# Optimization experiments

Hardware: AMD Instinct MI355X
Metric: run time of the kernel (lower is better)

Reference implementation:

```python
import jax, jax.numpy as jnp
import numpy as np

N_HEADS = 4
TAU = 0.1

def _ln(x, w, b):
    m = jnp.mean(x, axis=-1, keepdims=True)
    v = jnp.mean(jnp.square(x - m), axis=-1, keepdims=True)
    return (x - m) / jnp.sqrt(v + 1e-6) * w + b

def _l2norm(x):
    # torch F.normalize(dim=1): x / max(||x||_2, 1e-12)
    n = jnp.linalg.norm(x, axis=1, keepdims=True)
    return x / jnp.maximum(n, 1e-12)

def _sincos_pe(T, dim):
    pos = jnp.arange(T, dtype=jnp.float32)[:, None]
    div = jnp.exp(jnp.arange(0, dim, 2, dtype=jnp.float32) * (-np.log(10000.0) / dim))
    ang = pos * div[None, :]
    # interleave: even indices sin, odd indices cos
    return jnp.stack([jnp.sin(ang), jnp.cos(ang)], axis=-1).reshape(T, dim)

def reference(x, p1_w, p1_b, pln1_w, pln1_b, p2_w, pln2_w, pln2_b,
              in_proj_w, in_proj_b, out_proj_w, out_proj_b,
              ln1_w, ln1_b, lin1_w, lin1_b, lin2_w, lin2_b, ln2_w, ln2_b, head_w):
    B, T, D = x.shape
    E = p2_w.shape[0]           # bottleneck_dim = 256
    H = N_HEADS
    hd = E // H
    # projector: Linear -> LN -> GELU -> Linear(no bias) -> LN
    h = jax.nn.gelu(_ln(x.reshape(B * T, D) @ p1_w.T + p1_b, pln1_w, pln1_b), approximate=False)
    h = _ln(h @ p2_w.T, pln2_w, pln2_b).reshape(B, T, E)
    h = h + _sincos_pe(T, E)[None]
    causal = jnp.tril(jnp.ones((T, T), dtype=bool))
    L = in_proj_w.shape[0]
    for i in range(L):  # post-norm TransformerEncoderLayer
        qkv = h @ in_proj_w[i].T + in_proj_b[i]        # [B,T,3E]
        q, k, v = jnp.split(qkv, 3, axis=-1)
        q = q.reshape(B, T, H, hd).transpose(0, 2, 1, 3)
        k = k.reshape(B, T, H, hd).transpose(0, 2, 1, 3)
        v = v.reshape(B, T, H, hd).transpose(0, 2, 1, 3)
        scores = jnp.einsum('bhtd,bhsd->bhts', q, k) / np.float32(np.sqrt(hd))
        scores = jnp.where(causal[None, None], scores, -jnp.inf)
        probs = jax.nn.softmax(scores, axis=-1)        # materialized attn probs (eager path)
        attn = jnp.einsum('bhts,bhsd->bhtd', probs, v).transpose(0, 2, 1, 3).reshape(B, T, E)
        attn = attn @ out_proj_w[i].T + out_proj_b[i]
        h = _ln(h + attn, ln1_w[i], ln1_b[i])
        ff = jax.nn.gelu(h @ lin1_w[i].T + lin1_b[i], approximate=False) @ lin2_w[i].T + lin2_b[i]
        h = _ln(h + ff, ln2_w[i], ln2_b[i])
    flat = _l2norm(h.reshape(B * T, E))
    wn = _l2norm(head_w)
    return (flat @ wn.T / TAU).reshape(B, T, -1)

def setup_inputs() -> dict:
    key = jax.random.key(0)
    ks = jax.random.split(key, 8)
    B, T, D, E, HID, CLS, L = 2048, 20, 2048, 256, 1024, 1000, 2
    s = 0.02
    def w(k, shape):
        return jax.random.normal(k, shape, jnp.float32) * s
    return {
        'x': jax.random.normal(ks[0], (B, T, D), jnp.float32),
        'p1_w': w(ks[1], (HID, D)), 'p1_b': jnp.zeros((HID,), jnp.float32),
        'pln1_w': jnp.ones((HID,), jnp.float32), 'pln1_b': jnp.zeros((HID,), jnp.float32),
        'p2_w': w(ks[2], (E, HID)),
        'pln2_w': jnp.ones((E,), jnp.float32), 'pln2_b': jnp.zeros((E,), jnp.float32),
        'in_proj_w': w(ks[3], (L, 3 * E, E)), 'in_proj_b': jnp.zeros((L, 3 * E), jnp.float32),
        'out_proj_w': w(ks[4], (L, E, E)), 'out_proj_b': jnp.zeros((L, E), jnp.float32),
        'ln1_w': jnp.ones((L, E), jnp.float32), 'ln1_b': jnp.zeros((L, E), jnp.float32),
        'lin1_w': w(ks[5], (L, 4 * E, E)), 'lin1_b': jnp.zeros((L, 4 * E), jnp.float32),
        'lin2_w': w(ks[6], (L, E, 4 * E)), 'lin2_b': jnp.zeros((L, E), jnp.float32),
        'ln2_w': jnp.ones((L, E), jnp.float32), 'ln2_b': jnp.zeros((L, E), jnp.float32),
        'head_w': w(ks[7], (CLS, E)),
    }
```

## Files before the change

kernel.cpp:

```cpp
#include <hip/hip_runtime.h>
#include <math.h>

#define CDIV(a,b) (((a)+(b)-1)/(b))

typedef unsigned short bfu;
typedef short   s16x8 __attribute__((ext_vector_type(8)));
typedef float   f32x4 __attribute__((ext_vector_type(4)));

#define GLOAD16(gp, lp) __builtin_amdgcn_global_load_lds( \
    (const __attribute__((address_space(1))) void*)(gp),  \
    (__attribute__((address_space(3))) void*)(lp), 16, 0, 0)

static __device__ __forceinline__ float gelu_exact(float x) {
    return 0.5f * x * (1.0f + erff(x * 0.7071067811865475f));
}
static __device__ __forceinline__ bfu f2bf(float x) {
    unsigned int u = __float_as_uint(x);
    unsigned int r = u + 0x7fffu + ((u >> 16) & 1u);
    return (bfu)(r >> 16);
}
static __device__ __forceinline__ float bf2f(bfu b) {
    return __uint_as_float(((unsigned int)b) << 16);
}
static __device__ __forceinline__ float wave_sum(float v) {
    #pragma unroll
    for (int off = 32; off; off >>= 1) v += __shfl_xor(v, off, 64);
    return v;
}

__global__ __launch_bounds__(256)
void cvt_kernel(const float* __restrict__ in, bfu* __restrict__ out, int n4)
{
    int i = blockIdx.x * 256 + threadIdx.x;
    const int stride = gridDim.x * 256;
    for (; i < n4; i += stride) {
        float4 f = ((const float4*)in)[i];
        ushort4 o;
        o.x = f2bf(f.x); o.y = f2bf(f.y); o.z = f2bf(f.z); o.w = f2bf(f.w);
        ((ushort4*)out)[i] = o;
    }
}

__global__ __launch_bounds__(256)
void cvt6_kernel(const float* __restrict__ s0, const float* __restrict__ s1,
                 const float* __restrict__ s2, const float* __restrict__ s3,
                 const float* __restrict__ s4, const float* __restrict__ s5,
                 bfu* __restrict__ dst)
{
    const int c0 = 524288;
    const int c1 = c0 + 65536;
    const int c2 = c1 + 98304;
    const int c3 = c2 + 32768;
    const int c4 = c3 + 131072;
    const int c5 = c4 + 131072;
    int i = blockIdx.x * 256 + threadIdx.x;
    const int stride = gridDim.x * 256;
    for (; i < c5; i += stride) {
        const float* s; int base;
        if      (i < c0) { s = s0; base = 0;  }
        else if (i < c1) { s = s1; base = c0; }
        else if (i < c2) { s = s2; base = c1; }
        else if (i < c3) { s = s3; base = c2; }
        else if (i < c4) { s = s4; base = c3; }
        else             { s = s5; base = c4; }
        float4 f = ((const float4*)s)[i - base];
        ushort4 o;
        o.x = f2bf(f.x); o.y = f2bf(f.y); o.z = f2bf(f.z); o.w = f2bf(f.w);
        ((ushort4*)dst)[i] = o;
    }
}

__global__ __launch_bounds__(256)
void pe_kernel(float* __restrict__ pe)
{
    const int t = blockIdx.x;
    const int c = threadIdx.x;
    const float div = expf((float)(c & ~1) * (-9.210340371976184f / 256.0f));
    const float ang = (float)t * div;
    pe[t * 256 + c] = (c & 1) ? cosf(ang) : sinf(ang);
}

template<bool GELU_EP, bool OUT_BF16>
__global__ __launch_bounds__(256)
void mfma_gemm(const bfu* __restrict__ A, const bfu* __restrict__ W,
               const float* __restrict__ bias, void* __restrict__ Cv,
               int M, int N, int K, float scale, int ntx)
{
    __shared__ bfu As[128 * 32];
    __shared__ bfu Ws[128 * 32];

    const int tid = threadIdx.x;
    const int nwg = gridDim.x;
    const int lid = (nwg & 7) ? (int)blockIdx.x
                              : ((int)blockIdx.x & 7) * (nwg >> 3) + ((int)blockIdx.x >> 3);
    const int row0 = (lid / ntx) * 128;
    const int col0 = (lid % ntx) * 128;

    const int lane = tid & 63;
    const int wave = tid >> 6;
    const int wm = (wave >> 1) * 64;
    const int wn = (wave & 1) * 64;
    const int fr = lane & 15;
    const int fk = (lane >> 4) * 8;

    const int lrow = lane >> 2;
    const int lk   = (lane & 3) * 8;
    const bfu* al0 = A + (size_t)(row0 + wave * 32 + lrow) * K + lk;
    const bfu* al1 = al0 + (size_t)16 * K;
    const bfu* wl0 = W + (size_t)(col0 + wave * 32 + lrow) * K + lk;
    const bfu* wl1 = wl0 + (size_t)16 * K;
    bfu* ad0 = &As[(wave * 2    ) * 512];
    bfu* ad1 = &As[(wave * 2 + 1) * 512];
    bfu* wd0 = &Ws[(wave * 2    ) * 512];
    bfu* wd1 = &Ws[(wave * 2 + 1) * 512];

    f32x4 acc[4][4];
    #pragma unroll
    for (int i = 0; i < 4; ++i)
        #pragma unroll
        for (int j = 0; j < 4; ++j) acc[i][j] = (f32x4)0.f;

    for (int k0 = 0; k0 < K; k0 += 32) {
        GLOAD16(al0 + k0, ad0);
        GLOAD16(al1 + k0, ad1);
        GLOAD16(wl0 + k0, wd0);
        GLOAD16(wl1 + k0, wd1);
        __syncthreads();

        s16x8 af[4], wf[4];
        #pragma unroll
        for (int i = 0; i < 4; ++i) af[i] = *(const s16x8*)&As[(wm + 16*i + fr) * 32 + fk];
        #pragma unroll
        for (int j = 0; j < 4; ++j) wf[j] = *(const s16x8*)&Ws[(wn + 16*j + fr) * 32 + fk];

        #pragma unroll
        for (int i = 0; i < 4; ++i)
            #pragma unroll
            for (int j = 0; j < 4; ++j)
                acc[i][j] = __builtin_amdgcn_mfma_f32_16x16x32_bf16(af[i], wf[j], acc[i][j], 0, 0, 0);
        __syncthreads();
    }

    #pragma unroll
    for (int i = 0; i < 4; ++i) {
        const int r = row0 + wm + 16 * i + (lane >> 4) * 4;
        #pragma unroll
        for (int j = 0; j < 4; ++j) {
            const int c = col0 + wn + 16 * j + fr;
            if (c < N) {
                const float bsum = bias ? bias[c] : 0.f;
                #pragma unroll
                for (int rr = 0; rr < 4; ++rr) {
                    float v = acc[i][j][rr] + bsum;
                    if (GELU_EP) v = gelu_exact(v);
                    v *= scale;
                    if (OUT_BF16) ((bfu*)Cv)[(size_t)(r + rr) * N + c] = f2bf(v);
                    else          ((float*)Cv)[(size_t)(r + rr) * N + c] = v;
                }
            }
        }
    }
}

template<bool GELU_EP, bool OUT_BF16>
__global__ __launch_bounds__(512, 2)
void mfma_gemm256(const bfu* __restrict__ A, const bfu* __restrict__ W,
                  const float* __restrict__ bias, void* __restrict__ Cv,
                  int M, int N, int K, float scale, int ntx)
{
    __shared__ bfu lds[2][2][8192];

    const int tid  = threadIdx.x;
    const int lane = tid & 63;
    const int wv   = tid >> 6;
    const int nwg  = gridDim.x;
    const int lid  = (nwg & 7) ? (int)blockIdx.x
                               : ((int)blockIdx.x & 7) * (nwg >> 3) + ((int)blockIdx.x >> 3);
    const int row0 = (lid / ntx) * 256;
    const int col0 = (lid % ntx) * 256;

    const int srow = wv * 16 + (lane >> 2);
    const int sk   = ((lane & 3) ^ ((lane >> 2) & 3)) * 8;
    const bfu* aS0 = A + (size_t)(row0 + srow)       * K + sk;
    const bfu* aS1 = A + (size_t)(row0 + srow + 128) * K + sk;
    const bfu* wS0 = W + (size_t)(col0 + srow)       * K + sk;
    const bfu* wS1 = W + (size_t)(col0 + srow + 128) * K + sk;
    const int dOff = wv * 512;

    const int wr = wv >> 2, wc = wv & 3;
    const int fr = lane & 15;
    const int slot = (((lane >> 4) ^ (fr & 3))) * 8;

    f32x4 acc[8][4];
    #pragma unroll
    for (int i = 0; i < 8; ++i)
        #pragma unroll
        for (int j = 0; j < 4; ++j) acc[i][j] = (f32x4)0.f;

    const int nt = K >> 5;

#define STAGE256(b_, t_) do { \
    const size_t ko_ = (size_t)(t_) * 32; \
    GLOAD16(aS0 + ko_, &lds[b_][0][dOff]); \
    GLOAD16(aS1 + ko_, &lds[b_][0][4096 + dOff]); \
    GLOAD16(wS0 + ko_, &lds[b_][1][dOff]); \
    GLOAD16(wS1 + ko_, &lds[b_][1][4096 + dOff]); \
} while (0)

    STAGE256(0, 0);
    STAGE256(1, 1);

    int cur = 0;
    for (int t = 0; t < nt; ++t) {
        if (t + 1 < nt) asm volatile("s_waitcnt vmcnt(4)" ::: "memory");
        else            asm volatile("s_waitcnt vmcnt(0)" ::: "memory");
        asm volatile("s_barrier" ::: "memory");

        const bfu* Ab = lds[cur][0];
        const bfu* Wb = lds[cur][1];

        s16x8 bfr[4], afr[8];
        #pragma unroll
        for (int j = 0; j < 4; ++j)
            bfr[j] = *(const s16x8*)&Wb[(wc * 64 + j * 16 + fr) * 32 + slot];
        #pragma unroll
        for (int i = 0; i < 4; ++i)
            afr[i] = *(const s16x8*)&Ab[(wr * 128 + i * 16 + fr) * 32 + slot];

        __builtin_amdgcn_s_setprio(1);
        #pragma unroll
        for (int i = 0; i < 4; ++i)
            #pragma unroll
            for (int j = 0; j < 4; ++j)
                acc[i][j] = __builtin_amdgcn_mfma_f32_16x16x32_bf16(afr[i], bfr[j], acc[i][j], 0, 0, 0);
        __builtin_amdgcn_s_setprio(0);

        #pragma unroll
        for (int i = 4; i < 8; ++i)
            afr[i] = *(const s16x8*)&Ab[(wr * 128 + i * 16 + fr) * 32 + slot];

        __builtin_amdgcn_s_setprio(1);
        #pragma unroll
        for (int i = 4; i < 8; ++i)
            #pragma unroll
            for (int j = 0; j < 4; ++j)
                acc[i][j] = __builtin_amdgcn_mfma_f32_16x16x32_bf16(afr[i], bfr[j], acc[i][j], 0, 0, 0);
        __builtin_amdgcn_s_setprio(0);

        asm volatile("s_barrier" ::: "memory");
        if (t + 2 < nt) STAGE256(cur, t + 2);
        cur ^= 1;
    }
#undef STAGE256

    #pragma unroll
    for (int i = 0; i < 8; ++i) {
        const int r = row0 + wr * 128 + 16 * i + (lane >> 4) * 4;
        #pragma unroll
        for (int j = 0; j < 4; ++j) {
            const int c = col0 + wc * 64 + 16 * j + fr;
            if (c < N) {
                const float bsum = bias ? bias[c] : 0.f;
                #pragma unroll
                for (int rr = 0; rr < 4; ++rr) {
                    float v = acc[i][j][rr] + bsum;
                    if (GELU_EP) v = gelu_exact(v);
                    v *= scale;
                    if (OUT_BF16) ((bfu*)Cv)[(size_t)(r + rr) * N + c] = f2bf(v);
                    else          ((float*)Cv)[(size_t)(r + rr) * N + c] = v;
                }
            }
        }
    }
}

__global__ __launch_bounds__(256)
void ln1024_kernel(const bfu* __restrict__ X, const float* __restrict__ w,
                   const float* __restrict__ b, bfu* __restrict__ Y)
{
    __shared__ float sbuf[4];
    const int row = blockIdx.x;
    const bfu* xr = X + (size_t)row * 1024;

    ushort4 t4 = *(const ushort4*)(xr + threadIdx.x * 4);
    float v[4] = {bf2f(t4.x), bf2f(t4.y), bf2f(t4.z), bf2f(t4.w)};

    float s = v[0] + v[1] + v[2] + v[3];
    s = wave_sum(s);
    const int lane = threadIdx.x & 63, wid = threadIdx.x >> 6;
    if (lane == 0) sbuf[wid] = s;
    __syncthreads();
    const float mean = (sbuf[0] + sbuf[1] + sbuf[2] + sbuf[3]) * (1.f / 1024.f);

    float q = 0.f;
    #pragma unroll
    for (int j = 0; j < 4; ++j) { float d = v[j] - mean; q += d * d; }
    q = wave_sum(q);
    __syncthreads();
    if (lane == 0) sbuf[wid] = q;
    __syncthreads();
    const float var  = (sbuf[0] + sbuf[1] + sbuf[2] + sbuf[3]) * (1.f / 1024.f);
    const float rstd = rsqrtf(var + 1e-6f);

    ushort4 o;
    #pragma unroll
    for (int j = 0; j < 4; ++j) {
        const int c = threadIdx.x * 4 + j;
        float y = gelu_exact((v[j] - mean) * rstd * w[c] + b[c]);
        ((bfu*)&o)[j] = f2bf(y);
    }
    *(ushort4*)(Y + (size_t)row * 1024 + threadIdx.x * 4) = o;
}

template<bool ADD_PE, bool RES>
__global__ __launch_bounds__(256)
void ln256_kernel(const float* __restrict__ X, const float* __restrict__ R,
                  const float* __restrict__ w, const float* __restrict__ b,
                  const float* __restrict__ pe, float* __restrict__ Yf,
                  bfu* __restrict__ Yb, int T)
{
    const int row  = blockIdx.x * 4 + (threadIdx.x >> 6);
    const int lane = threadIdx.x & 63;

    float4 v = *(const float4*)(X + (size_t)row * 256 + lane * 4);
    if (RES) {
        float4 r4 = *(const float4*)(R + (size_t)row * 256 + lane * 4);
        v.x += r4.x; v.y += r4.y; v.z += r4.z; v.w += r4.w;
    }

    const float mean = wave_sum(v.x + v.y + v.z + v.w) * (1.f / 256.f);
    float q = (v.x-mean)*(v.x-mean) + (v.y-mean)*(v.y-mean)
            + (v.z-mean)*(v.z-mean) + (v.w-mean)*(v.w-mean);
    const float rstd = rsqrtf(wave_sum(q) * (1.f / 256.f) + 1e-6f);

    const float4 w4 = *(const float4*)(w + lane * 4);
    const float4 b4 = *(const float4*)(b + lane * 4);
    float y[4] = {(v.x-mean)*rstd*w4.x + b4.x, (v.y-mean)*rstd*w4.y + b4.y,
                  (v.z-mean)*rstd*w4.z + b4.z, (v.w-mean)*rstd*w4.w + b4.w};
    if (ADD_PE) {
        const float4 p4 = *(const float4*)(pe + (size_t)(row % T) * 256 + lane * 4);
        y[0] += p4.x; y[1] += p4.y; y[2] += p4.z; y[3] += p4.w;
    }

    if (Yf) *(float4*)(Yf + (size_t)row * 256 + lane * 4) = float4{y[0], y[1], y[2], y[3]};
    if (Yb) {
        ushort4 o = {f2bf(y[0]), f2bf(y[1]), f2bf(y[2]), f2bf(y[3])};
        *(ushort4*)(Yb + (size_t)row * 256 + lane * 4) = o;
    }
}

__global__ __launch_bounds__(64)
void attn_kernel(const bfu* __restrict__ qkv, bfu* __restrict__ out,
                 int B, int T, int H)
{
    __shared__ float qs[20][65];
    __shared__ float ks[20][65];
    __shared__ float vs[20][65];
    __shared__ float probs[64];

    const int blk = blockIdx.x;
    const int b = blk / H;
    const int h = blk % H;
    const int tid = threadIdx.x;

    for (int t = 0; t < T; ++t) {
        const bfu* base = qkv + (size_t)(b * T + t) * 768 + h * 64 + tid;
        qs[t][tid] = bf2f(base[0]);
        ks[t][tid] = bf2f(base[256]);
        vs[t][tid] = bf2f(base[512]);
    }
    __syncthreads();

    for (int t = 0; t < T; ++t) {
        float sc = -INFINITY;
        if (tid <= t) {
            float s = 0.f;
            #pragma unroll
            for (int d = 0; d < 64; ++d) s = fmaf(qs[t][d], ks[tid][d], s);
            sc = s * 0.125f;
        }
        float m = sc;
        #pragma unroll
        for (int off = 32; off; off >>= 1) m = fmaxf(m, __shfl_xor(m, off, 64));
        float p = (tid <= t) ? expf(sc - m) : 0.f;
        float sum = p;
        #pragma unroll
        for (int off = 32; off; off >>= 1) sum += __shfl_xor(sum, off, 64);
        p /= sum;
        probs[tid] = p;
        __syncthreads();

        float o = 0.f;
        for (int s = 0; s <= t; ++s) o = fmaf(probs[s], vs[s][tid], o);
        out[(size_t)(b * T + t) * 256 + h * 64 + tid] = f2bf(o);
        __syncthreads();
    }
}

__global__ __launch_bounds__(256)
void l2norm_kernel(const float* __restrict__ X, bfu* __restrict__ Y)
{
    const int row  = blockIdx.x * 4 + (threadIdx.x >> 6);
    const int lane = threadIdx.x & 63;
    float4 v = *(const float4*)(X + (size_t)row * 256 + lane * 4);
    float n = sqrtf(wave_sum(v.x*v.x + v.y*v.y + v.z*v.z + v.w*v.w));
    n = 1.f / fmaxf(n, 1e-12f);
    ushort4 o = {f2bf(v.x*n), f2bf(v.y*n), f2bf(v.z*n), f2bf(v.w*n)};
    *(ushort4*)(Y + (size_t)row * 256 + lane * 4) = o;
}

extern "C" void kernel_launch(void* const* d_in, const int* in_sizes, int n_in,
                              void* d_out, int out_size, void* d_ws, size_t ws_size,
                              hipStream_t stream)
{
    const float* x         = (const float*)d_in[0];
    const float* p1_w      = (const float*)d_in[1];
    const float* p1_b      = (const float*)d_in[2];
    const float* pln1_w    = (const float*)d_in[3];
    const float* pln1_b    = (const float*)d_in[4];
    const float* p2_w      = (const float*)d_in[5];
    const float* pln2_w    = (const float*)d_in[6];
    const float* pln2_b    = (const float*)d_in[7];
    const float* in_proj_w = (const float*)d_in[8];
    const float* in_proj_b = (const float*)d_in[9];
    const float* out_proj_w= (const float*)d_in[10];
    const float* out_proj_b= (const float*)d_in[11];
    const float* ln1_w     = (const float*)d_in[12];
    const float* ln1_b     = (const float*)d_in[13];
    const float* lin1_w    = (const float*)d_in[14];
    const float* lin1_b    = (const float*)d_in[15];
    const float* lin2_w    = (const float*)d_in[16];
    const float* lin2_b    = (const float*)d_in[17];
    const float* ln2_w     = (const float*)d_in[18];
    const float* ln2_b     = (const float*)d_in[19];
    const float* head_w    = (const float*)d_in[20];

    const int B = 2048, T = 20, E = 256, HID = 1024, CLS = 1000, L = 2, H = 4;
    const int M = B * T;
    const int D = 2048;

    char* p = (char*)d_ws;
    bfu*   xb     = (bfu*)p;    p += (size_t)M * D * 2;
    bfu*   h1b    = (bfu*)p;    p += (size_t)M * HID * 2;
    bfu*   wblk   = (bfu*)p;    p += (size_t)3932160 * 2;
    bfu*   wnb    = (bfu*)p;    p += (size_t)1024 * E * 2;
    float* pe     = (float*)p;  p += (size_t)T * 256 * 4;

    char* q = (char*)xb;
    float* h      = (float*)q;  q += (size_t)M * E * 4;
    float* ffout  = (float*)q;  q += (size_t)M * E * 4;
    bfu*   hb     = (bfu*)q;    q += (size_t)M * E * 2;
    bfu*   abf    = (bfu*)q;    q += (size_t)M * E * 2;

    bfu* p1wb  = wblk;
    bfu* p2wb  = p1wb  + (size_t)HID * D;
    bfu* qkvwb = p2wb  + (size_t)E * HID;
    bfu* outwb = qkvwb + (size_t)L * 3 * E * E;
    bfu* l1wb  = outwb + (size_t)L * E * E;
    bfu* l2wb  = l1wb  + (size_t)L * 4 * E * E;

    float* out   = (float*)d_out;
    bfu*   qkvb  = (bfu*)d_out;
    float* attnp = (float*)d_out;

    cvt_kernel<<<2048, 256, 0, stream>>>(x, xb, M * D / 4);
    cvt6_kernel<<<2048, 256, 0, stream>>>(p1_w, p2_w, in_proj_w, out_proj_w, lin1_w, lin2_w, wblk);
    pe_kernel<<<T, 256, 0, stream>>>(pe);

    mfma_gemm256<false, true><<<dim3((M/256) * (HID/256)), 512, 0, stream>>>(
        xb, p1wb, p1_b, h1b, M, HID, D, 1.f, HID/256);
    ln1024_kernel<<<M, 256, 0, stream>>>(h1b, pln1_w, pln1_b, h1b);
    mfma_gemm256<false, false><<<dim3(M/256), 512, 0, stream>>>(
        h1b, p2wb, nullptr, h, M, E, HID, 1.f, 1);
    ln256_kernel<true, false><<<M/4, 256, 0, stream>>>(
        h, nullptr, pln2_w, pln2_b, pe, h, hb, T);

    for (int l = 0; l < L; ++l) {
        mfma_gemm<false, true><<<dim3(6 * (M/128)), 256, 0, stream>>>(
            hb, qkvwb + (size_t)l * 3*E*E, in_proj_b + (size_t)l * 3*E, qkvb, M, 3*E, E, 1.f, 6);
        attn_kernel<<<B * H, 64, 0, stream>>>(qkvb, abf, B, T, H);
        mfma_gemm<false, false><<<dim3(2 * (M/128)), 256, 0, stream>>>(
            abf, outwb + (size_t)l * E*E, out_proj_b + (size_t)l * E, attnp, M, E, E, 1.f, 2);
        ln256_kernel<false, true><<<M/4, 256, 0, stream>>>(
            h, attnp, ln1_w + (size_t)l * E, ln1_b + (size_t)l * E, nullptr, h, hb, T);
        mfma_gemm<true, true><<<dim3(8 * (M/128)), 256, 0, stream>>>(
            hb, l1wb + (size_t)l * 4*E*E, lin1_b + (size_t)l * 4*E, h1b, M, HID, E, 1.f, 8);
        mfma_gemm256<false, false><<<dim3(M/256), 512, 0, stream>>>(
            h1b, l2wb + (size_t)l * E*4*E, lin2_b + (size_t)l * E, ffout, M, E, HID, 1.f, 1);
        ln256_kernel<false, true><<<M/4, 256, 0, stream>>>(
            h, ffout, ln2_w + (size_t)l * E, ln2_b + (size_t)l * E, nullptr, h, hb, T);
    }

    l2norm_kernel<<<M/4, 256, 0, stream>>>(h, hb);
    l2norm_kernel<<<CLS/4, 256, 0, stream>>>(head_w, wnb);
    mfma_gemm<false, false><<<dim3(8 * (M/128)), 256, 0, stream>>>(
        hb, wnb, nullptr, out, M, CLS, E, 10.f, 8);
}
```

Baseline: 1.257 ms.

## Fuse residual+LayerNorm into N=256 GEMM epilogues and use 256-tile GEMM everywhere

Adds a GEMM kernel whose block covers 128 full rows of the 256-wide output. Its epilogue adds bias and the residual, reduces mean and variance across waves through LDS, then writes the normalized fp32 and bf16 activations in place. This replaces the separate p2, out_proj and lin2 GEMMs plus their ln256 passes, removing the round trips of the intermediate fp32 buffers. The remaining 128x128 GEMM launches (QKV, lin1, classifier head) move to the double-buffered 256x256 kernel. Risks: variance is now computed as E[x^2]-mean^2, which is less stable, and the grids for the N=256 GEMMs are smaller.

```diff
diff --git a/kernel.cpp b/kernel.cpp
--- a/kernel.cpp
+++ b/kernel.cpp
@@ -81,88 +81,6 @@
 }
 
 template<bool GELU_EP, bool OUT_BF16>
-__global__ __launch_bounds__(256)
-void mfma_gemm(const bfu* __restrict__ A, const bfu* __restrict__ W,
-               const float* __restrict__ bias, void* __restrict__ Cv,
-               int M, int N, int K, float scale, int ntx)
-{
-    __shared__ bfu As[128 * 32];
-    __shared__ bfu Ws[128 * 32];
-
-    const int tid = threadIdx.x;
-    const int nwg = gridDim.x;
-    const int lid = (nwg & 7) ? (int)blockIdx.x
-                              : ((int)blockIdx.x & 7) * (nwg >> 3) + ((int)blockIdx.x >> 3);
-    const int row0 = (lid / ntx) * 128;
-    const int col0 = (lid % ntx) * 128;
-
-    const int lane = tid & 63;
-    const int wave = tid >> 6;
-    const int wm = (wave >> 1) * 64;
-    const int wn = (wave & 1) * 64;
-    const int fr = lane & 15;
-    const int fk = (lane >> 4) * 8;
-
-    const int lrow = lane >> 2;
-    const int lk   = (lane & 3) * 8;
-    const bfu* al0 = A + (size_t)(row0 + wave * 32 + lrow) * K + lk;
-    const bfu* al1 = al0 + (size_t)16 * K;
-    const bfu* wl0 = W + (size_t)(col0 + wave * 32 + lrow) * K + lk;
-    const bfu* wl1 = wl0 + (size_t)16 * K;
-    bfu* ad0 = &As[(wave * 2    ) * 512];
-    bfu* ad1 = &As[(wave * 2 + 1) * 512];
-    bfu* wd0 = &Ws[(wave * 2    ) * 512];
-    bfu* wd1 = &Ws[(wave * 2 + 1) * 512];
-
-    f32x4 acc[4][4];
-    #pragma unroll
-    for (int i = 0; i < 4; ++i)
-        #pragma unroll
-        for (int j = 0; j < 4; ++j) acc[i][j] = (f32x4)0.f;
-
-    for (int k0 = 0; k0 < K; k0 += 32) {
-        GLOAD16(al0 + k0, ad0);
-        GLOAD16(al1 + k0, ad1);
-        GLOAD16(wl0 + k0, wd0);
-        GLOAD16(wl1 + k0, wd1);
-        __syncthreads();
-
-        s16x8 af[4], wf[4];
-        #pragma unroll
-        for (int i = 0; i < 4; ++i) af[i] = *(const s16x8*)&As[(wm + 16*i + fr) * 32 + fk];
-        #pragma unroll
-        for (int j = 0; j < 4; ++j) wf[j] = *(const s16x8*)&Ws[(wn + 16*j + fr) * 32 + fk];
-
-        #pragma unroll
-        for (int i = 0; i < 4; ++i)
-            #pragma unroll
-            for (int j = 0; j < 4; ++j)
-                acc[i][j] = __builtin_amdgcn_mfma_f32_16x16x32_bf16(af[i], wf[j], acc[i][j], 0, 0, 0);
-        __syncthreads();
-    }
-
-    #pragma unroll
-    for (int i = 0; i < 4; ++i) {
-        const int r = row0 + wm + 16 * i + (lane >> 4) * 4;
-        #pragma unroll
-        for (int j = 0; j < 4; ++j) {
-            const int c = col0 + wn + 16 * j + fr;
-            if (c < N) {
-                const float bsum = bias ? bias[c] : 0.f;
-                #pragma unroll
-                for (int rr = 0; rr < 4; ++rr) {
-                    float v = acc[i][j][rr] + bsum;
-                    if (GELU_EP) v = gelu_exact(v);
-                    v *= scale;
-                    if (OUT_BF16) ((bfu*)Cv)[(size_t)(r + rr) * N + c] = f2bf(v);
-                    else          ((float*)Cv)[(size_t)(r + rr) * N + c] = v;
-                }
-            }
-        }
-    }
-}
-
-template<bool GELU_EP, bool OUT_BF16>
 __global__ __launch_bounds__(512, 2)
 void mfma_gemm256(const bfu* __restrict__ A, const bfu* __restrict__ W,
                   const float* __restrict__ bias, void* __restrict__ Cv,
@@ -274,6 +192,153 @@
     }
 }
 
+template<bool RES, bool ADD_PE>
+__global__ __launch_bounds__(512, 2)
+void mfma_gemm_ln(const bfu* __restrict__ A, const bfu* __restrict__ W,
+                  const float* __restrict__ bias, const float* __restrict__ R,
+                  const float* __restrict__ lnw, const float* __restrict__ lnb,
+                  const float* __restrict__ pe, float* __restrict__ Yf,
+                  bfu* __restrict__ Yb, int M, int K, int T)
+{
+    __shared__ bfu ldsA[2][4096];
+    __shared__ bfu ldsW[2][8192];
+
+    const int tid  = threadIdx.x;
+    const int lane = tid & 63;
+    const int wv   = tid >> 6;
+    const int nwg  = gridDim.x;
+    const int lid  = (nwg & 7) ? (int)blockIdx.x
+                               : ((int)blockIdx.x & 7) * (nwg >> 3) + ((int)blockIdx.x >> 3);
+    const int row0 = lid * 128;
+
+    const int srow = wv * 16 + (lane >> 2);
+    const int sk   = ((lane & 3) ^ ((lane >> 2) & 3)) * 8;
+    const bfu* aS  = A + (size_t)(row0 + srow) * K + sk;
+    const bfu* wS0 = W + (size_t)(srow)        * K + sk;
+    const bfu* wS1 = W + (size_t)(srow + 128)  * K + sk;
+    const int dOff = wv * 512;
+
+    const int wr = wv >> 2, wc = wv & 3;
+    const int fr = lane & 15;
+    const int g4 = lane >> 4;
+    const int slot = ((g4 ^ (fr & 3))) * 8;
+
+    f32x4 acc[4][4];
+    #pragma unroll
+    for (int i = 0; i < 4; ++i)
+        #pragma unroll
+        for (int j = 0; j < 4; ++j) acc[i][j] = (f32x4)0.f;
+
+    const int nt = K >> 5;
+
+#define STAGELN(b_, t_) do { \
+    const size_t ko_ = (size_t)(t_) * 32; \
+    GLOAD16(aS  + ko_, &ldsA[b_][dOff]); \
+    GLOAD16(wS0 + ko_, &ldsW[b_][dOff]); \
+    GLOAD16(wS1 + ko_, &ldsW[b_][4096 + dOff]); \
+} while (0)
+
+    STAGELN(0, 0);
+    STAGELN(1, 1);
+
+    int cur = 0;
+    for (int t = 0; t < nt; ++t) {
+        if (t + 1 < nt) asm volatile("s_waitcnt vmcnt(3)" ::: "memory");
+        else            asm volatile("s_waitcnt vmcnt(0)" ::: "memory");
+        asm volatile("s_barrier" ::: "memory");
+
+        const bfu* Ab = ldsA[cur];
+        const bfu* Wb = ldsW[cur];
+
+        s16x8 bfr[4], afr[4];
+        #pragma unroll
+        for (int j = 0; j < 4; ++j)
+            bfr[j] = *(const s16x8*)&Wb[(wc * 64 + j * 16 + fr) * 32 + slot];
+        #pragma unroll
+        for (int i = 0; i < 4; ++i)
+            afr[i] = *(const s16x8*)&Ab[(wr * 64 + i * 16 + fr) * 32 + slot];
+
+        __builtin_amdgcn_s_setprio(1);
+        #pragma unroll
+        for (int i = 0; i < 4; ++i)
+            #pragma unroll
+            for (int j = 0; j < 4; ++j)
+                acc[i][j] = __builtin_amdgcn_mfma_f32_16x16x32_bf16(afr[i], bfr[j], acc[i][j], 0, 0, 0);
+        __builtin_amdgcn_s_setprio(0);
+
+        asm volatile("s_barrier" ::: "memory");
+        if (t + 2 < nt) STAGELN(cur, t + 2);
+        cur ^= 1;
+    }
+#undef STAGELN
+
+    float* red   = (float*)ldsA;
+    float* stats = red + 1024;
+
+    float bj[4];
+    #pragma unroll
+    for (int j = 0; j < 4; ++j)
+        bj[j] = bias ? bias[wc * 64 + j * 16 + fr] : 0.f;
+
+    #pragma unroll
+    for (int i = 0; i < 4; ++i) {
+        #pragma unroll
+        for (int rr = 0; rr < 4; ++rr) {
+            const int rl = wr * 64 + i * 16 + g4 * 4 + rr;
+            const size_t r = (size_t)(row0 + rl);
+            float s = 0.f, q = 0.f;
+            #pragma unroll
+            for (int j = 0; j < 4; ++j) {
+                float v = acc[i][j][rr] + bj[j];
+                if (RES) v += R[r * 256 + (wc * 64 + j * 16 + fr)];
+                acc[i][j][rr] = v;
+                s += v; q += v * v;
+            }
+            #pragma unroll
+            for (int off = 1; off < 16; off <<= 1) {
+                s += __shfl_xor(s, off, 64);
+                q += __shfl_xor(q, off, 64);
+            }
+            if (fr == 0) { red[rl * 4 + wc] = s; red[512 + rl * 4 + wc] = q; }
+        }
+    }
+    __syncthreads();
+    if (tid < 128) {
+        const float s = red[tid*4+0] + red[tid*4+1] + red[tid*4+2] + red[tid*4+3];
+        const float q = red[512+tid*4+0] + red[512+tid*4+1] + red[512+tid*4+2] + red[512+tid*4+3];
+        const float mean = s * (1.f / 256.f);
+        const float var  = q * (1.f / 256.f) - mean * mean;
+        stats[tid]       = mean;
+        stats[128 + tid] = rsqrtf(var + 1e-6f);
+    }
+    __syncthreads();
+
+    float lw[4], lb[4];
+    #pragma unroll
+    for (int j = 0; j < 4; ++j) {
+        const int c = wc * 64 + j * 16 + fr;
+        lw[j] = lnw[c]; lb[j] = lnb[c];
+    }
+    #pragma unroll
+    for (int i = 0; i < 4; ++i) {
+        #pragma unroll
+        for (int rr = 0; rr < 4; ++rr) {
+            const int rl = wr * 64 + i * 16 + g4 * 4 + rr;
+            const size_t r = (size_t)(row0 + rl);
+            const float mean = stats[rl], rstd = stats[128 + rl];
+            const int tmod = (int)(r % (size_t)T);
+            #pragma unroll
+            for (int j = 0; j < 4; ++j) {
+                const int c = wc * 64 + j * 16 + fr;
+                float y = (acc[i][j][rr] - mean) * rstd * lw[j] + lb[j];
+                if (ADD_PE) y += pe[tmod * 256 + c];
+                Yf[r * 256 + c] = y;
+                Yb[r * 256 + c] = f2bf(y);
+            }
+        }
+    }
+}
+
 __global__ __launch_bounds__(256)
 void ln1024_kernel(const bfu* __restrict__ X, const float* __restrict__ w,
                    const float* __restrict__ b, bfu* __restrict__ Y)
@@ -310,43 +375,6 @@
         ((bfu*)&o)[j] = f2bf(y);
     }
     *(ushort4*)(Y + (size_t)row * 1024 + threadIdx.x * 4) = o;
-}
-
-template<bool ADD_PE, bool RES>
-__global__ __launch_bounds__(256)
-void ln256_kernel(const float* __restrict__ X, const float* __restrict__ R,
-                  const float* __restrict__ w, const float* __restrict__ b,
-                  const float* __restrict__ pe, float* __restrict__ Yf,
-                  bfu* __restrict__ Yb, int T)
-{
-    const int row  = blockIdx.x * 4 + (threadIdx.x >> 6);
-    const int lane = threadIdx.x & 63;
-
-    float4 v = *(const float4*)(X + (size_t)row * 256 + lane * 4);
-    if (RES) {
-        float4 r4 = *(const float4*)(R + (size_t)row * 256 + lane * 4);
-        v.x += r4.x; v.y += r4.y; v.z += r4.z; v.w += r4.w;
-    }
-
-    const float mean = wave_sum(v.x + v.y + v.z + v.w) * (1.f / 256.f);
-    float q = (v.x-mean)*(v.x-mean) + (v.y-mean)*(v.y-mean)
-            + (v.z-mean)*(v.z-mean) + (v.w-mean)*(v.w-mean);
-    const float rstd = rsqrtf(wave_sum(q) * (1.f / 256.f) + 1e-6f);
-
-    const float4 w4 = *(const float4*)(w + lane * 4);
-    const float4 b4 = *(const float4*)(b + lane * 4);
-    float y[4] = {(v.x-mean)*rstd*w4.x + b4.x, (v.y-mean)*rstd*w4.y + b4.y,
-                  (v.z-mean)*rstd*w4.z + b4.z, (v.w-mean)*rstd*w4.w + b4.w};
-    if (ADD_PE) {
-        const float4 p4 = *(const float4*)(pe + (size_t)(row % T) * 256 + lane * 4);
-        y[0] += p4.x; y[1] += p4.y; y[2] += p4.z; y[3] += p4.w;
-    }
-
-    if (Yf) *(float4*)(Yf + (size_t)row * 256 + lane * 4) = float4{y[0], y[1], y[2], y[3]};
-    if (Yb) {
-        ushort4 o = {f2bf(y[0]), f2bf(y[1]), f2bf(y[2]), f2bf(y[3])};
-        *(ushort4*)(Yb + (size_t)row * 256 + lane * 4) = o;
-    }
 }
 
 __global__ __launch_bounds__(64)
@@ -448,7 +476,6 @@
 
     char* q = (char*)xb;
     float* h      = (float*)q;  q += (size_t)M * E * 4;
-    float* ffout  = (float*)q;  q += (size_t)M * E * 4;
     bfu*   hb     = (bfu*)q;    q += (size_t)M * E * 2;
     bfu*   abf    = (bfu*)q;    q += (size_t)M * E * 2;
 
@@ -461,7 +488,6 @@
 
     float* out   = (float*)d_out;
     bfu*   qkvb  = (bfu*)d_out;
-    float* attnp = (float*)d_out;
 
     cvt_kernel<<<2048, 256, 0, stream>>>(x, xb, M * D / 4);
     cvt6_kernel<<<2048, 256, 0, stream>>>(p1_w, p2_w, in_proj_w, out_proj_w, lin1_w, lin2_w, wblk);
@@ -470,29 +496,25 @@
     mfma_gemm256<false, true><<<dim3((M/256) * (HID/256)), 512, 0, stream>>>(
         xb, p1wb, p1_b, h1b, M, HID, D, 1.f, HID/256);
     ln1024_kernel<<<M, 256, 0, stream>>>(h1b, pln1_w, pln1_b, h1b);
-    mfma_gemm256<false, false><<<dim3(M/256), 512, 0, stream>>>(
-        h1b, p2wb, nullptr, h, M, E, HID, 1.f, 1);
-    ln256_kernel<true, false><<<M/4, 256, 0, stream>>>(
-        h, nullptr, pln2_w, pln2_b, pe, h, hb, T);
+    mfma_gemm_ln<false, true><<<dim3(M/128), 512, 0, stream>>>(
+        h1b, p2wb, nullptr, nullptr, pln2_w, pln2_b, pe, h, hb, M, HID, T);
 
     for (int l = 0; l < L; ++l) {
-        mfma_gemm<false, true><<<dim3(6 * (M/128)), 256, 0, stream>>>(
-            hb, qkvwb + (size_t)l * 3*E*E, in_proj_b + (size_t)l * 3*E, qkvb, M, 3*E, E, 1.f, 6);
+        mfma_gemm256<false, true><<<dim3(3 * (M/256)), 512, 0, stream>>>(
+            hb, qkvwb + (size_t)l * 3*E*E, in_proj_b + (size_t)l * 3*E, qkvb, M, 3*E, E, 1.f, 3);
         attn_kernel<<<B * H, 64, 0, stream>>>(qkvb, abf, B, T, H);
-        mfma_gemm<false, false><<<dim3(2 * (M/128)), 256, 0, stream>>>(
-            abf, outwb + (size_t)l * E*E, out_proj_b + (size_t)l * E, attnp, M, E, E, 1.f, 2);
-        ln256_kernel<false, true><<<M/4, 256, 0, stream>>>(
-            h, attnp, ln1_w + (size_t)l * E, ln1_b + (size_t)l * E, nullptr, h, hb, T);
-        mfma_gemm<true, true><<<dim3(8 * (M/128)), 256, 0, stream>>>(
-            hb, l1wb + (size_t)l * 4*E*E, lin1_b + (size_t)l * 4*E, h1b, M, HID, E, 1.f, 8);
-        mfma_gemm256<false, false><<<dim3(M/256), 512, 0, stream>>>(
-            h1b, l2wb + (size_t)l * E*4*E, lin2_b + (size_t)l * E, ffout, M, E, HID, 1.f, 1);
-        ln256_kernel<false, true><<<M/4, 256, 0, stream>>>(
-            h, ffout, ln2_w + (size_t)l * E, ln2_b + (size_t)l * E, nullptr, h, hb, T);
+        mfma_gemm_ln<true, false><<<dim3(M/128), 512, 0, stream>>>(
+            abf, outwb + (size_t)l * E*E, out_proj_b + (size_t)l * E, h,
+            ln1_w + (size_t)l * E, ln1_b + (size_t)l * E, nullptr, h, hb, M, E, T);
+        mfma_gemm256<true, true><<<dim3(4 * (M/256)), 512, 0, stream>>>(
+            hb, l1wb + (size_t)l * 4*E*E, lin1_b + (size_t)l * 4*E, h1b, M, HID, E, 1.f, 4);
+        mfma_gemm_ln<true, false><<<dim3(M/128), 512, 0, stream>>>(
+            h1b, l2wb + (size_t)l * E*4*E, lin2_b + (size_t)l * E, h,
+            ln2_w + (size_t)l * E, ln2_b + (size_t)l * E, nullptr, h, hb, M, HID, T);
     }
 
     l2norm_kernel<<<M/4, 256, 0, stream>>>(h, hb);
     l2norm_kernel<<<CLS/4, 256, 0, stream>>>(head_w, wnb);
-    mfma_gemm<false, false><<<dim3(8 * (M/128)), 256, 0, stream>>>(
-        hb, wnb, nullptr, out, M, CLS, E, 10.f, 8);
-}
+    mfma_gemm256<false, false><<<dim3(4 * (M/256)), 512, 0, stream>>>(
+        hb, wnb, nullptr, out, M, CLS, E, 10.f, 4);
+}
```

New measurement: 1.234 ms. About the same (-1.9%).
